# Kernel optimization log

Hardware: AMD Instinct MI355X
Metric: run time of the kernel (lower is better)

Reference implementation:

```python
import jax, jax.numpy as jnp
import numpy as np

V, E, H = 1024, 256, 512
B, L = 2048, 32
DEC_T = 7
LN_EPS = 1e-5


def _lstm(xg, Whh, h0, c0, reverse=False):
    # xg: (T, B, 4H) precomputed input gates (x @ Wih^T + b_ih + b_hh)
    def step(carry, g_in):
        h, c = carry
        g = g_in + h @ Whh.T
        i, f, gg, o = jnp.split(g, 4, axis=-1)  # torch gate order: i, f, g, o
        c = jax.nn.sigmoid(f) * c + jax.nn.sigmoid(i) * jnp.tanh(gg)
        h = jax.nn.sigmoid(o) * jnp.tanh(c)
        return (h, c), h
    (hT, cT), outs = jax.lax.scan(step, (h0, c0), xg, reverse=reverse)
    return outs, hT


def _ln(x, g, b):
    m = jnp.mean(x, axis=-1, keepdims=True)
    v = jnp.var(x, axis=-1, keepdims=True)
    return (x - m) * jax.lax.rsqrt(v + LN_EPS) * g + b


def setup_inputs() -> dict:
    key = jax.random.key(0)
    ks = jax.random.split(key, 24)
    s_e = 1.0 / np.sqrt(H)
    d = {
        'features': jax.random.randint(ks[0], (B, L), 0, V, dtype=jnp.int32),
        'eps': jax.random.normal(ks[1], (B, 1, H), dtype=jnp.float32),
        'emb': jax.random.normal(ks[2], (V, E), dtype=jnp.float32),
        'enc_Wih_f': jax.random.uniform(ks[3], (4 * H, E), minval=-s_e, maxval=s_e),
        'enc_Whh_f': jax.random.uniform(ks[4], (4 * H, H), minval=-s_e, maxval=s_e),
        'enc_bih_f': jax.random.uniform(ks[5], (4 * H,), minval=-s_e, maxval=s_e),
        'enc_bhh_f': jax.random.uniform(ks[6], (4 * H,), minval=-s_e, maxval=s_e),
        'enc_Wih_b': jax.random.uniform(ks[7], (4 * H, E), minval=-s_e, maxval=s_e),
        'enc_Whh_b': jax.random.uniform(ks[8], (4 * H, H), minval=-s_e, maxval=s_e),
        'enc_bih_b': jax.random.uniform(ks[9], (4 * H,), minval=-s_e, maxval=s_e),
        'enc_bhh_b': jax.random.uniform(ks[10], (4 * H,), minval=-s_e, maxval=s_e),
        'dec_Wih': jax.random.uniform(ks[11], (4 * H, E), minval=-s_e, maxval=s_e),
        'dec_Whh': jax.random.uniform(ks[12], (4 * H, H), minval=-s_e, maxval=s_e),
        'dec_bih': jax.random.uniform(ks[13], (4 * H,), minval=-s_e, maxval=s_e),
        'dec_bhh': jax.random.uniform(ks[14], (4 * H,), minval=-s_e, maxval=s_e),
        'mu_ln_g': jnp.ones((2 * H,)), 'mu_ln_b': jnp.zeros((2 * H,)),
        'mu_W': jax.random.uniform(ks[15], (H, 2 * H), minval=-s_e, maxval=s_e),
        'mu_b': jax.random.uniform(ks[16], (H,), minval=-s_e, maxval=s_e),
        'lv_ln_g': jnp.ones((2 * H,)), 'lv_ln_b': jnp.zeros((2 * H,)),
        'lv_W': jax.random.uniform(ks[17], (H, 2 * H), minval=-s_e, maxval=s_e) * 0.1,
        'lv_b': jax.random.uniform(ks[18], (H,), minval=-s_e, maxval=s_e),
        'ff_W': jax.random.uniform(ks[19], (V, H), minval=-s_e, maxval=s_e),
        'ff_b': jax.random.uniform(ks[20], (V,), minval=-s_e, maxval=s_e),
    }
    d['emb'] = d['emb'].at[0].set(0.0)  # padding_idx=0
    return d


def reference(features, eps, emb,
              enc_Wih_f, enc_Whh_f, enc_bih_f, enc_bhh_f,
              enc_Wih_b, enc_Whh_b, enc_bih_b, enc_bhh_b,
              dec_Wih, dec_Whh, dec_bih, dec_bhh,
              mu_ln_g, mu_ln_b, mu_W, mu_b,
              lv_ln_g, lv_ln_b, lv_W, lv_b,
              ff_W, ff_b):
    emb_eff = emb.at[0].set(0.0)  # enforce zero padding row (and zero its grad)
    x = emb_eff[features]  # (B, L, E)
    b, l, _ = x.shape
    h = dec_Whh.shape[1]
    h0 = jnp.zeros((b, h), x.dtype)

    # Bidirectional encoder: gate preactivations per direction, (L, B, 4H)
    xg_f = (jnp.einsum('ble,ge->blg', x, enc_Wih_f) + enc_bih_f + enc_bhh_f).transpose(1, 0, 2)
    xg_b = (jnp.einsum('ble,ge->blg', x, enc_Wih_b) + enc_bih_b + enc_bhh_b).transpose(1, 0, 2)
    _, hT_f = _lstm(xg_f, enc_Whh_f, h0, h0, reverse=False)
    _, hT_b = _lstm(xg_b, enc_Whh_b, h0, h0, reverse=True)
    new_h = jnp.concatenate([hT_f, hT_b], axis=-1)[:, None, :]  # (B, 1, 2H)

    mu = _ln(new_h, mu_ln_g, mu_ln_b) @ mu_W.T + mu_b          # (B, 1, H)
    logvar = _ln(new_h, lv_ln_g, lv_ln_b) @ lv_W.T + lv_b      # (B, 1, H)
    z = mu + jnp.sqrt(jnp.exp(logvar)) * eps                   # (B, 1, H)

    # Decoder: input is zeros -> input gates are just biases, broadcast over T
    gd = jnp.broadcast_to((dec_bih + dec_bhh)[None, None, :], (DEC_T, b, 4 * h))
    z0 = z[:, 0, :]
    outs, _ = _lstm(gd, dec_Whh, z0, z0, reverse=False)        # (T, B, H)
    features_hat = outs.transpose(1, 0, 2) @ ff_W.T + ff_b     # (B, T, V)
    return features, features_hat, mu, logvar
```

## Files before the change

### kernel.cpp

```cpp
#include <hip/hip_runtime.h>
#include <hip/hip_bf16.h>
#include <math.h>

#define B_ 2048
#define L_ 32
#define V_ 1024
#define E_ 256
#define H_ 512
#define DEC_T_ 7
#define NA_ (B_ * H_)

typedef unsigned short u16;
typedef unsigned int u32;
using bf16x8 = __attribute__((ext_vector_type(8))) short;
using f32x4  = __attribute__((ext_vector_type(4))) float;

#define WAITVM(n) asm volatile("s_waitcnt vmcnt(" #n ")" ::: "memory")
#define SCHED0()  __builtin_amdgcn_sched_barrier(0)

__device__ __forceinline__ u16 f2b(float f) {
  union { float f; u32 i; } x; x.f = f;
  u32 r = x.i + 0x7FFFu + ((x.i >> 16) & 1u);
  return (u16)(r >> 16);
}
__device__ __forceinline__ float b2f(u16 u) {
  union { u32 i; float f; } x; x.i = ((u32)u) << 16; return x.f;
}
__device__ __forceinline__ float sigm(float x) { return 1.f / (1.f + __expf(-x)); }
__device__ __forceinline__ float tanhfast(float x) {
  const float xx = fminf(fmaxf(x, -15.f), 15.f);
  const float e = __expf(2.f * xx);
  return (e - 1.f) / (e + 1.f);
}

__device__ __forceinline__ void gl_lds16(const void* g, void* l) {
  __builtin_amdgcn_global_load_lds((const __attribute__((address_space(1))) u32*)g,
                                   (__attribute__((address_space(3))) u32*)l, 16, 0, 0);
}
__device__ __forceinline__ void gl_lds16c(const void* g, void* l) {
  __builtin_amdgcn_global_load_lds((const __attribute__((address_space(1))) u32*)g,
                                   (__attribute__((address_space(3))) u32*)l, 16, 0, 1);
}

__device__ __forceinline__ void gbar_mono(unsigned* cnt, unsigned target) {
  __syncthreads();
  if (threadIdx.x == 0) {
    __hip_atomic_fetch_add(cnt, 1u, __ATOMIC_RELAXED, __HIP_MEMORY_SCOPE_AGENT);
    for (int it = 0; it < (1 << 20); ++it) {
      if (__hip_atomic_load(cnt, __ATOMIC_RELAXED, __HIP_MEMORY_SCOPE_AGENT) >= target) break;
      __builtin_amdgcn_s_sleep(2);
    }
  }
  asm volatile("" ::: "memory");
  __syncthreads();
}

__launch_bounds__(512, 1)
__global__ void enc_persist_k(const int* __restrict__ feat, const u16* __restrict__ emb,
                              const u16* __restrict__ Wf, const u16* __restrict__ Wbk,
                              const float* __restrict__ bsf, const float* __restrict__ bsb,
                              u16* hfa, u16* hfb, u16* hba, u16* hbb,
                              unsigned* bar) {
  __shared__ u16 Wlds[64 * 768];
  __shared__ u16 At[2][512 * 32];
  const int tid = threadIdx.x;
  const int lane = tid & 63, wave = tid >> 6;
  const int bid = blockIdx.x;
  const int xcd = bid & 7;
  const int dir = xcd >> 2;
  const int m0 = (xcd & 3) * 512;
  const int j0 = (bid >> 3) * 64;
  const u16* W = dir ? Wbk : Wf;
  const float* bsum = dir ? bsb : bsf;
  u16* hA = dir ? hba : hfa;
  u16* hB = dir ? hbb : hfb;
  unsigned* cnt = bar + xcd * 64;

  const int lr = lane & 15;
  const int swk = ((lane >> 4) ^ ((lane >> 1) & 3)) * 8;
  const int csrc = ((lane & 3) ^ ((lane >> 3) & 3)) * 8;
  const int xw = (lr >> 1) & 7;

  {
    const int row = tid >> 3;
    const u16* wsrc = W + (j0 + row) * (E_ + H_);
    u16* wdst = Wlds + row * 768;
    const int xr = (row >> 1) & 7;
#pragma unroll
    for (int q = 0; q < 12; ++q) {
      const int ck = (tid & 7) + q * 8;
      *(uint4*)(wdst + (ck ^ xr) * 8) = *(const uint4*)(wsrc + ck * 8);
    }
  }

  const int arow = lane >> 2;
  const int mbase = m0 + wave * 64;
  const int nblk = j0 >> 2;
  const int jsub = (lane >> 4) * 4;

  float creg[4][4] = {};
  __syncthreads();

  for (int s = 0; s < L_; ++s) {
    const int tc = dir ? (L_ - 1 - s) : s;
    int tok[4];
#pragma unroll
    for (int q = 0; q < 4; ++q)
      tok[q] = feat[(mbase + q * 16 + arow) * L_ + tc];
    const u16* hin = (s & 1) ? hB : hA;
    u16* hout = (s & 1) ? hA : hB;

    if (s) gbar_mono(cnt, 32u * (unsigned)s);

    auto stage = [&](int kt, int buf) {
      const int k0 = kt << 5;
      u16* ad = &At[buf][(wave * 64) * 32];
#pragma unroll
      for (int q = 0; q < 4; ++q) {
        u16* dst = ad + (q * 16) * 32;
        if (k0 < E_) gl_lds16(emb + tok[q] * E_ + k0 + csrc, dst);
        else gl_lds16c(hin + (mbase + q * 16 + arow) * H_ + (k0 - E_) + csrc, dst);
      }
    };

    f32x4 acc[4][4] = {};
    stage(0, 0);
    __syncthreads();
    int cur = 0;
    for (int kt = 0; kt < 24; ++kt) {
      if (kt + 1 < 24) stage(kt + 1, cur ^ 1);
      const u16* Ab = &At[cur][0];
      const int pk = ((kt * 4 + (lane >> 4)) ^ xw) * 8;
      bf16x8 af[4], bb[4];
#pragma unroll
      for (int t = 0; t < 4; ++t)
        af[t] = *(const bf16x8*)(Wlds + (t * 16 + lr) * 768 + pk);
#pragma unroll
      for (int t = 0; t < 4; ++t)
        bb[t] = *(const bf16x8*)(Ab + (wave * 64 + t * 16 + lr) * 32 + swk);
#pragma unroll
      for (int i = 0; i < 4; ++i)
#pragma unroll
        for (int j = 0; j < 4; ++j)
          acc[i][j] = __builtin_amdgcn_mfma_f32_16x16x32_bf16(af[i], bb[j], acc[i][j], 0, 0, 0);
      __syncthreads();
      cur ^= 1;
    }

    u16* hlds = &At[0][0];
#pragma unroll
    for (int i = 0; i < 4; ++i) {
      const int jb = j0 + i * 16 + jsub;
      const float4 bs = *(const float4*)(bsum + jb);
      const int nloc = i * 4 + (lane >> 4);
#pragma unroll
      for (int j = 0; j < 4; ++j) {
        const int mloc = wave * 64 + j * 16 + lr;
        const float gi = acc[i][j][0] + bs.x;
        const float gf = acc[i][j][1] + bs.y;
        const float gg = acc[i][j][2] + bs.z;
        const float go = acc[i][j][3] + bs.w;
        const float cn = sigm(gf) * creg[i][j] + sigm(gi) * tanhfast(gg);
        creg[i][j] = cn;
        hlds[mloc * 20 + nloc] = f2b(sigm(go) * tanhfast(cn));
      }
    }
    __syncthreads();
#pragma unroll
    for (int cc = 0; cc < 2; ++cc) {
      const int ch = tid + cc * 512;
      const int row = ch >> 1, half = ch & 1;
      *(uint4*)(hout + (m0 + row) * H_ + nblk + half * 8) =
          *(const uint4*)(hlds + row * 20 + half * 8);
    }
    __syncthreads();
  }
}

__launch_bounds__(256, 2)
__global__ void dec_persist_k(const u16* __restrict__ Wd, const float* __restrict__ bsd,
                              const u16* __restrict__ dz, const float* __restrict__ dcc,
                              u16* dech, unsigned* bar) {
  __shared__ u16 sh[4 * 8192];
  const int tid = threadIdx.x;
  const int lane = tid & 63, wave = tid >> 6;
  const int wr = wave & 1, wc = wave >> 1;
  const int bid = blockIdx.x;
  const int xcd = bid & 7;
  const int l = xcd * 32 + (bid >> 3);
  const int j0 = (l & 15) * 128;
  const int m0 = ((l >> 5) * 2 + ((l >> 4) & 1)) * 128;
  unsigned* cnt = bar + (8 + xcd) * 64;

  const int lr = lane & 15;
  const int swk = ((lane >> 4) ^ ((lane >> 1) & 3)) * 8;
  const int srow = wave * 32 + (lane >> 2);
  const int csrc = ((lane & 3) ^ ((lane >> 3) & 3)) * 8;
  const u16* wsrc0 = Wd + (j0 + srow) * H_ + csrc;
  const u16* wsrc1 = wsrc0 + 16 * H_;
  const int sw32 = (wave * 32) * 32;
  u16* hlds = sh;
  const int jb_base = j0 + wr * 64 + (lane >> 4) * 4;
  const int n0 = j0 >> 2;

  float creg[4][4];
#pragma unroll
  for (int i = 0; i < 4; ++i) {
    const int n = (jb_base + i * 16) >> 2;
#pragma unroll
    for (int j = 0; j < 4; ++j)
      creg[i][j] = dcc[n * B_ + (m0 + wc * 64 + j * 16 + lr)];
  }
  WAITVM(0);

  for (int t = 0; t < DEC_T_; ++t) {
    const u16* hin = t ? (dech + (long)(t - 1) * NA_) : dz;
    u16* hout = dech + (long)t * NA_;
    const u16* h0 = hin + (m0 + srow) * H_ + csrc;
    const u16* h1 = h0 + 16 * H_;

    if (t) gbar_mono(cnt, 32u * (unsigned)t);

    auto stage = [&](int kt) {
      const int b = kt & 3;
      const int k0 = kt << 5;
      u16* wd = sh + b * 8192 + sw32;
      u16* ad = sh + b * 8192 + 4096 + sw32;
      gl_lds16(wsrc0 + k0, wd);
      gl_lds16(wsrc1 + k0, wd + 512);
      gl_lds16c(h0 + k0, ad);
      gl_lds16c(h1 + k0, ad + 512);
    };

    f32x4 acc[4][4] = {};
    auto compute = [&](int kt) {
      const u16* Wb2 = sh + (kt & 3) * 8192;
      const u16* Ab2 = Wb2 + 4096;
      bf16x8 af[4], bb[4];
#pragma unroll
      for (int tt = 0; tt < 4; ++tt) {
        af[tt] = *(const bf16x8*)(Wb2 + (wr * 64 + tt * 16 + lr) * 32 + swk);
        bb[tt] = *(const bf16x8*)(Ab2 + (wc * 64 + tt * 16 + lr) * 32 + swk);
      }
#pragma unroll
      for (int i = 0; i < 4; ++i)
#pragma unroll
        for (int j = 0; j < 4; ++j)
          acc[i][j] = __builtin_amdgcn_mfma_f32_16x16x32_bf16(af[i], bb[j], acc[i][j], 0, 0, 0);
    };

    stage(0); stage(1); stage(2);
    for (int kt = 0; kt <= 16 - 4; ++kt) {
      WAITVM(8); SCHED0();
      __builtin_amdgcn_s_barrier(); SCHED0();
      stage(kt + 3);
      compute(kt);
    }
    WAITVM(8); SCHED0(); __builtin_amdgcn_s_barrier(); SCHED0(); compute(13);
    WAITVM(4); SCHED0(); __builtin_amdgcn_s_barrier(); SCHED0(); compute(14);
    WAITVM(0); SCHED0(); __builtin_amdgcn_s_barrier(); SCHED0(); compute(15);

#pragma unroll
    for (int i = 0; i < 4; ++i) {
      const int jb = jb_base + i * 16;
      const float4 bs = *(const float4*)(bsd + jb);
      const int nloc = (jb - j0) >> 2;
#pragma unroll
      for (int j = 0; j < 4; ++j) {
        const int mloc = wc * 64 + j * 16 + lr;
        const float gi = acc[i][j][0] + bs.x;
        const float gf = acc[i][j][1] + bs.y;
        const float gg = acc[i][j][2] + bs.z;
        const float go = acc[i][j][3] + bs.w;
        const float cn = sigm(gf) * creg[i][j] + sigm(gi) * tanhfast(gg);
        creg[i][j] = cn;
        hlds[mloc * 40 + nloc] = f2b(sigm(go) * tanhfast(cn));
      }
    }
    __syncthreads();
#pragma unroll
    for (int cc = 0; cc < 2; ++cc) {
      const int ch = tid + cc * 256;
      const int row = ch >> 2, cpos = (ch & 3) * 8;
      *(uint4*)(hout + (m0 + row) * H_ + n0 + cpos) = *(const uint4*)(hlds + row * 40 + cpos);
    }
  }
}

struct OP {
  const u16* A; const u16* W; const float* bias;
  float* Cf; int ldc; int K;
};

__launch_bounds__(256)
__global__ void out_mfma_k(OP p0, OP p1) {
  OP p = blockIdx.z ? p1 : p0;
  __shared__ u16 Ws[2][128 * 32];
  __shared__ u16 As[2][128 * 32];
  const int tid = threadIdx.x;
  const int lane = tid & 63, wave = tid >> 6;
  const int wr = wave & 1, wc = wave >> 1;
  const int v0 = blockIdx.x * 128, m0 = blockIdx.y * 128;
  const int lr = lane & 15;
  const int swk = ((lane >> 4) ^ ((lane >> 1) & 3)) * 8;

  const int srow = wave * 32 + (lane >> 2);
  const int csrc = ((lane & 3) ^ ((lane >> 3) & 3)) * 8;
  const u16* wsrc0 = p.W + (v0 + srow) * p.K + csrc;
  const u16* wsrc1 = wsrc0 + 16 * p.K;
  const u16* asrc0 = p.A + (m0 + srow) * p.K + csrc;
  const u16* asrc1 = asrc0 + 16 * p.K;
  u16* wdst0 = &Ws[0][(wave * 32) * 32];
  u16* wdst1 = wdst0 + 16 * 32;
  u16* adst0 = &As[0][(wave * 32) * 32];
  u16* adst1 = adst0 + 16 * 32;

  f32x4 acc[4][4] = {};
  const int NT = p.K >> 5;

  auto stage = [&](int kt, int buf) {
    const int k0 = kt << 5;
    const int bo = buf * 4096;
    gl_lds16(wsrc0 + k0, wdst0 + bo);
    gl_lds16(wsrc1 + k0, wdst1 + bo);
    gl_lds16(asrc0 + k0, adst0 + bo);
    gl_lds16(asrc1 + k0, adst1 + bo);
  };

  stage(0, 0);
  __syncthreads();
  int cur = 0;
  for (int kt = 0; kt < NT; ++kt) {
    if (kt + 1 < NT) stage(kt + 1, cur ^ 1);
    const u16* Wb = &Ws[cur][0];
    const u16* Ab = &As[cur][0];
    bf16x8 aa[4], bb[4];
#pragma unroll
    for (int t = 0; t < 4; ++t) {
      aa[t] = *(const bf16x8*)(Ab + (wr * 64 + t * 16 + lr) * 32 + swk);
      bb[t] = *(const bf16x8*)(Wb + (wc * 64 + t * 16 + lr) * 32 + swk);
    }
#pragma unroll
    for (int i = 0; i < 4; ++i)
#pragma unroll
      for (int j = 0; j < 4; ++j)
        acc[i][j] = __builtin_amdgcn_mfma_f32_16x16x32_bf16(aa[i], bb[j], acc[i][j], 0, 0, 0);
    __syncthreads();
    cur ^= 1;
  }

#pragma unroll
  for (int j = 0; j < 4; ++j) {
    const int v = v0 + wc * 64 + j * 16 + lr;
    const float bv = p.bias[v];
#pragma unroll
    for (int i = 0; i < 4; ++i) {
      const int mb = m0 + wr * 64 + i * 16 + (lane >> 4) * 4;
#pragma unroll
      for (int r = 0; r < 4; ++r) {
        const int m = mb + r;
        const float val = acc[i][j][r] + bv;
        if (p.ldc) p.Cf[m * p.ldc + v] = val;
        else p.Cf[(m & (B_ - 1)) * (DEC_T_ * V_) + (m >> 11) * V_ + v] = val;
      }
    }
  }
}

__global__ void prep_gates_k(const float* Wih, const float* Whh,
                             const float* b1, const float* b2,
                             u16* Wout, float* bsum, int KI, int K) {
  const int j = blockIdx.y;
  const int k = blockIdx.x * 256 + threadIdx.x;
  const int worig = (j & 3) * H_ + (j >> 2);
  const float v = (k < KI) ? Wih[worig * KI + k] : Whh[worig * H_ + (k - KI)];
  Wout[(long)j * K + k] = f2b(v);
  if (k == 0) bsum[j] = b1[worig] + b2[worig];
}

__global__ void cast_k(const float* s, u16* d) {
  const int i = blockIdx.x * 256 + threadIdx.x;
  d[i] = f2b(s[i]);
}

__global__ void init_k(u16* a, u16* b, unsigned* bar) {
  const int i = blockIdx.x * 256 + threadIdx.x;
  a[i] = 0; b[i] = 0;
  if (i < 1024) bar[i] = 0u;
}

__global__ void cast_feat_k(const int* f, float* o) {
  const int i = blockIdx.x * 256 + threadIdx.x;
  o[i] = b2f(f2b((float)f[i]));
}

__global__ void ln_k(const u16* hf, const u16* hb,
                     const float* g0, const float* b0,
                     const float* g1, const float* b1,
                     u16* A0, u16* A1) {
  const int b = blockIdx.x, t = threadIdx.x;
  const int k4 = t * 4;
  const u16* src = (k4 < H_) ? (hf + b * H_ + k4) : (hb + b * H_ + (k4 - H_));
  const ushort4 raw = *(const ushort4*)src;
  const float x0 = b2f(raw.x), x1 = b2f(raw.y), x2 = b2f(raw.z), x3 = b2f(raw.w);
  float s = x0 + x1 + x2 + x3;
  float sq = x0 * x0 + x1 * x1 + x2 * x2 + x3 * x3;
#pragma unroll
  for (int off = 32; off; off >>= 1) {
    s += __shfl_down(s, off);
    sq += __shfl_down(sq, off);
  }
  __shared__ float ss[4], ssq[4], smv[2];
  if ((t & 63) == 0) { ss[t >> 6] = s; ssq[t >> 6] = sq; }
  __syncthreads();
  if (t == 0) {
    const float S = ss[0] + ss[1] + ss[2] + ss[3];
    const float SQ = ssq[0] + ssq[1] + ssq[2] + ssq[3];
    const float m = S * (1.f / 1024.f);
    const float var = SQ * (1.f / 1024.f) - m * m;
    smv[0] = m; smv[1] = rsqrtf(var + 1e-5f);
  }
  __syncthreads();
  const float m = smv[0], rs = smv[1];
  const float4 ga = *(const float4*)(g0 + k4), ba = *(const float4*)(b0 + k4);
  const float4 gb = *(const float4*)(g1 + k4), bb = *(const float4*)(b1 + k4);
  ushort4 o0, o1;
  o0.x = f2b((x0 - m) * rs * ga.x + ba.x);
  o0.y = f2b((x1 - m) * rs * ga.y + ba.y);
  o0.z = f2b((x2 - m) * rs * ga.z + ba.z);
  o0.w = f2b((x3 - m) * rs * ga.w + ba.w);
  o1.x = f2b((x0 - m) * rs * gb.x + bb.x);
  o1.y = f2b((x1 - m) * rs * gb.y + bb.y);
  o1.z = f2b((x2 - m) * rs * gb.z + bb.z);
  o1.w = f2b((x3 - m) * rs * gb.w + bb.w);
  *(ushort4*)(A0 + b * 1024 + k4) = o0;
  *(ushort4*)(A1 + b * 1024 + k4) = o1;
}

__global__ void z_k(const float* mu, const float* lv, const float* eps,
                    u16* dz, float* dc) {
  const int i = blockIdx.x * 256 + threadIdx.x;
  const float z = mu[i] + __expf(0.5f * lv[i]) * eps[i];
  dz[i] = f2b(z);
  dc[(i & (H_ - 1)) * B_ + (i >> 9)] = z;
}

extern "C" void kernel_launch(void* const* d_in, const int* in_sizes, int n_in,
                              void* d_out, int out_size, void* d_ws, size_t ws_size,
                              hipStream_t stream) {
  const int*   features = (const int*)d_in[0];
  const float* eps      = (const float*)d_in[1];
  const float* emb      = (const float*)d_in[2];
  const float* eWih_f   = (const float*)d_in[3];
  const float* eWhh_f   = (const float*)d_in[4];
  const float* ebih_f   = (const float*)d_in[5];
  const float* ebhh_f   = (const float*)d_in[6];
  const float* eWih_b   = (const float*)d_in[7];
  const float* eWhh_b   = (const float*)d_in[8];
  const float* ebih_b   = (const float*)d_in[9];
  const float* ebhh_b   = (const float*)d_in[10];
  const float* dWhh     = (const float*)d_in[12];
  const float* dbih     = (const float*)d_in[13];
  const float* dbhh     = (const float*)d_in[14];
  const float* mu_ln_g  = (const float*)d_in[15];
  const float* mu_ln_b  = (const float*)d_in[16];
  const float* mu_W     = (const float*)d_in[17];
  const float* mu_b     = (const float*)d_in[18];
  const float* lv_ln_g  = (const float*)d_in[19];
  const float* lv_ln_b  = (const float*)d_in[20];
  const float* lv_W     = (const float*)d_in[21];
  const float* lv_b     = (const float*)d_in[22];
  const float* ff_W     = (const float*)d_in[23];
  const float* ff_b     = (const float*)d_in[24];

  float* of = (float*)d_out;
  float* o_feat = of;
  float* o_fh   = of + (B_ * L_);
  float* o_mu   = o_fh + (long)B_ * DEC_T_ * V_;
  float* o_lv   = o_mu + (long)B_ * H_;

  u16* hfa = (u16*)d_ws;
  u16* hba = hfa + NA_;
  u16* hfb = hba + NA_;
  u16* hbb = hfb + NA_;
  u16* Wenc_f = hbb + NA_;
  u16* Wenc_b = Wenc_f + 2048 * 768;
  u16* Wdec   = Wenc_b + 2048 * 768;
  u16* Wff    = Wdec + 2048 * 512;
  u16* Wmu    = Wff + 1024 * 512;
  u16* Wlv    = Wmu + 512 * 1024;
  u16* embb   = Wlv + 512 * 1024;
  float* bsum_f = (float*)(embb + V_ * E_);
  float* bsum_b = bsum_f + 2048;
  float* bsum_d = bsum_b + 2048;
  unsigned* bar = (unsigned*)(bsum_d + 2048);
  u16* dz     = (u16*)(bar + 1024);
  float* dc   = (float*)(dz + NA_);
  u16* An0    = hfb;
  u16* An1    = Wenc_f;
  u16* dech   = hfa;

  cast_feat_k<<<dim3(B_ * L_ / 256), dim3(256), 0, stream>>>(features, o_feat);
  init_k<<<dim3(NA_ / 256), dim3(256), 0, stream>>>(hfa, hba, bar);

  prep_gates_k<<<dim3(3, 2048), dim3(256), 0, stream>>>(eWih_f, eWhh_f, ebih_f, ebhh_f, Wenc_f, bsum_f, E_, E_ + H_);
  prep_gates_k<<<dim3(3, 2048), dim3(256), 0, stream>>>(eWih_b, eWhh_b, ebih_b, ebhh_b, Wenc_b, bsum_b, E_, E_ + H_);
  prep_gates_k<<<dim3(2, 2048), dim3(256), 0, stream>>>(nullptr, dWhh, dbih, dbhh, Wdec, bsum_d, 0, H_);
  cast_k<<<dim3(1024 * 512 / 256), dim3(256), 0, stream>>>(ff_W, Wff);
  cast_k<<<dim3(512 * 1024 / 256), dim3(256), 0, stream>>>(mu_W, Wmu);
  cast_k<<<dim3(512 * 1024 / 256), dim3(256), 0, stream>>>(lv_W, Wlv);
  cast_k<<<dim3(V_ * E_ / 256), dim3(256), 0, stream>>>(emb, embb);

  enc_persist_k<<<dim3(256), dim3(512), 0, stream>>>(
      features, embb, Wenc_f, Wenc_b, bsum_f, bsum_b,
      hfa, hfb, hba, hbb, bar);

  ln_k<<<dim3(B_), dim3(256), 0, stream>>>(hfa, hba, mu_ln_g, mu_ln_b, lv_ln_g, lv_ln_b, An0, An1);
  {
    OP pm{}, pl{};
    pm.A = An0; pm.W = Wmu; pm.bias = mu_b; pm.Cf = o_mu; pm.ldc = H_; pm.K = 2 * H_;
    pl = pm;
    pl.A = An1; pl.W = Wlv; pl.bias = lv_b; pl.Cf = o_lv;
    out_mfma_k<<<dim3(4, 16, 2), dim3(256), 0, stream>>>(pm, pl);
  }
  z_k<<<dim3(NA_ / 256), dim3(256), 0, stream>>>(o_mu, o_lv, eps, dz, dc);

  dec_persist_k<<<dim3(256), dim3(256), 0, stream>>>(Wdec, bsum_d, dz, dc, dech, bar);

  {
    OP po{};
    po.A = dech; po.W = Wff; po.bias = ff_b;
    po.Cf = o_fh; po.ldc = 0;
    po.K = H_;
    out_mfma_k<<<dim3(8, DEC_T_ * 16, 1), dim3(256), 0, stream>>>(po, po);
  }
}
```

Baseline: 1.057 ms.

## Give each wave private LDS staging and drop block barriers in persistent LSTM kernels

The encoder now stages activations into per-wave LDS buffers, so the K loop drops its per-step __syncthreads in favour of vmcnt/lgkmcnt waits. The grid barrier is deferred until after the embedding-part k-tiles, which read only the token embeddings, so input-projection work overlaps the wait for the other blocks' hidden states. The decoder is restructured to match: 512 threads per block, recurrent weights resident in LDS, and each wave owning 32 batch rows with wave-private staging. This removes intra-block barriers and repeated weight loads, at the cost of smaller per-wave tiles and the correctness risk of wave-local LDS reuse without block syncs.

```diff
diff --git a/kernel.cpp b/kernel.cpp
--- a/kernel.cpp
+++ b/kernel.cpp
@@ -16,6 +16,7 @@
 using f32x4  = __attribute__((ext_vector_type(4))) float;
 
 #define WAITVM(n) asm volatile("s_waitcnt vmcnt(" #n ")" ::: "memory")
+#define WAITLG0() asm volatile("s_waitcnt lgkmcnt(0)" ::: "memory")
 #define SCHED0()  __builtin_amdgcn_sched_barrier(0)
 
 __device__ __forceinline__ u16 f2b(float f) {
@@ -62,7 +63,7 @@
                               u16* hfa, u16* hfb, u16* hba, u16* hbb,
                               unsigned* bar) {
   __shared__ u16 Wlds[64 * 768];
-  __shared__ u16 At[2][512 * 32];
+  __shared__ u16 At[8][2][2048];
   const int tid = threadIdx.x;
   const int lane = tid & 63, wave = tid >> 6;
   const int bid = blockIdx.x;
@@ -76,10 +77,14 @@
   u16* hB = dir ? hbb : hfb;
   unsigned* cnt = bar + xcd * 64;
 
-  const int lr = lane & 15;
-  const int swk = ((lane >> 4) ^ ((lane >> 1) & 3)) * 8;
+  const int lr = lane & 15, hi = lane >> 4;
+  const int swk = (hi ^ ((lane >> 1) & 3)) * 8;
   const int csrc = ((lane & 3) ^ ((lane >> 3) & 3)) * 8;
   const int xw = (lr >> 1) & 7;
+  const int arow = lane >> 2;
+  const int mw0 = m0 + wave * 64;
+  const int n0 = j0 >> 2;
+  const int jsub = hi * 4;
 
   {
     const int row = tid >> 3;
@@ -92,12 +97,6 @@
       *(uint4*)(wdst + (ck ^ xr) * 8) = *(const uint4*)(wsrc + ck * 8);
     }
   }
-
-  const int arow = lane >> 2;
-  const int mbase = m0 + wave * 64;
-  const int nblk = j0 >> 2;
-  const int jsub = (lane >> 4) * 4;
-
   float creg[4][4] = {};
   __syncthreads();
 
@@ -106,183 +105,194 @@
     int tok[4];
 #pragma unroll
     for (int q = 0; q < 4; ++q)
-      tok[q] = feat[(mbase + q * 16 + arow) * L_ + tc];
+      tok[q] = feat[(mw0 + q * 16 + arow) * L_ + tc];
     const u16* hin = (s & 1) ? hB : hA;
     u16* hout = (s & 1) ? hA : hB;
 
-    if (s) gbar_mono(cnt, 32u * (unsigned)s);
-
     auto stage = [&](int kt, int buf) {
       const int k0 = kt << 5;
-      u16* ad = &At[buf][(wave * 64) * 32];
+      u16* ad = &At[wave][buf][0];
 #pragma unroll
       for (int q = 0; q < 4; ++q) {
         u16* dst = ad + (q * 16) * 32;
         if (k0 < E_) gl_lds16(emb + tok[q] * E_ + k0 + csrc, dst);
-        else gl_lds16c(hin + (mbase + q * 16 + arow) * H_ + (k0 - E_) + csrc, dst);
+        else gl_lds16c(hin + (mw0 + q * 16 + arow) * H_ + (k0 - E_) + csrc, dst);
       }
     };
 
     f32x4 acc[4][4] = {};
-    stage(0, 0);
-    __syncthreads();
-    int cur = 0;
-    for (int kt = 0; kt < 24; ++kt) {
-      if (kt + 1 < 24) stage(kt + 1, cur ^ 1);
-      const u16* Ab = &At[cur][0];
-      const int pk = ((kt * 4 + (lane >> 4)) ^ xw) * 8;
+    auto compute = [&](int kt) {
+      const int pk = ((kt * 4 + hi) ^ xw) * 8;
+      const u16* Ab = &At[wave][kt & 1][0];
       bf16x8 af[4], bb[4];
 #pragma unroll
       for (int t = 0; t < 4; ++t)
         af[t] = *(const bf16x8*)(Wlds + (t * 16 + lr) * 768 + pk);
 #pragma unroll
       for (int t = 0; t < 4; ++t)
-        bb[t] = *(const bf16x8*)(Ab + (wave * 64 + t * 16 + lr) * 32 + swk);
+        bb[t] = *(const bf16x8*)(Ab + (t * 16 + lr) * 32 + swk);
+      WAITLG0(); SCHED0();
+      if (kt + 2 < 24) stage(kt + 2, kt & 1);
 #pragma unroll
       for (int i = 0; i < 4; ++i)
 #pragma unroll
         for (int j = 0; j < 4; ++j)
           acc[i][j] = __builtin_amdgcn_mfma_f32_16x16x32_bf16(af[i], bb[j], acc[i][j], 0, 0, 0);
-      __syncthreads();
-      cur ^= 1;
-    }
-
-    u16* hlds = &At[0][0];
+    };
+
+    stage(0, 0); stage(1, 1);
+    for (int kt = 0; kt < 6; ++kt) {
+      WAITVM(4); SCHED0();
+      compute(kt);
+    }
+    if (s) gbar_mono(cnt, 32u * (unsigned)s);
+    for (int kt = 6; kt < 23; ++kt) {
+      WAITVM(4); SCHED0();
+      compute(kt);
+    }
+    WAITVM(0); SCHED0();
+    compute(23);
+
+    u16* hld = &At[wave][0][0];
 #pragma unroll
     for (int i = 0; i < 4; ++i) {
       const int jb = j0 + i * 16 + jsub;
       const float4 bs = *(const float4*)(bsum + jb);
-      const int nloc = i * 4 + (lane >> 4);
+      const int nloc = i * 4 + hi;
 #pragma unroll
       for (int j = 0; j < 4; ++j) {
-        const int mloc = wave * 64 + j * 16 + lr;
+        const int mloc = j * 16 + lr;
         const float gi = acc[i][j][0] + bs.x;
         const float gf = acc[i][j][1] + bs.y;
         const float gg = acc[i][j][2] + bs.z;
         const float go = acc[i][j][3] + bs.w;
         const float cn = sigm(gf) * creg[i][j] + sigm(gi) * tanhfast(gg);
         creg[i][j] = cn;
-        hlds[mloc * 20 + nloc] = f2b(sigm(go) * tanhfast(cn));
+        hld[mloc * 20 + nloc] = f2b(sigm(go) * tanhfast(cn));
       }
     }
-    __syncthreads();
-#pragma unroll
-    for (int cc = 0; cc < 2; ++cc) {
-      const int ch = tid + cc * 512;
-      const int row = ch >> 1, half = ch & 1;
-      *(uint4*)(hout + (m0 + row) * H_ + nblk + half * 8) =
-          *(const uint4*)(hlds + row * 20 + half * 8);
-    }
-    __syncthreads();
-  }
-}
-
-__launch_bounds__(256, 2)
+    WAITLG0(); SCHED0();
+#pragma unroll
+    for (int c = 0; c < 2; ++c) {
+      const int idx = lane + c * 64;
+      const int row = idx >> 1, half = idx & 1;
+      *(uint4*)(hout + (mw0 + row) * H_ + n0 + half * 8) =
+          *(const uint4*)(hld + row * 20 + half * 8);
+    }
+  }
+}
+
+__launch_bounds__(512, 1)
 __global__ void dec_persist_k(const u16* __restrict__ Wd, const float* __restrict__ bsd,
                               const u16* __restrict__ dz, const float* __restrict__ dcc,
                               u16* dech, unsigned* bar) {
-  __shared__ u16 sh[4 * 8192];
+  __shared__ u16 Wlds[64 * 512];
+  __shared__ u16 At[8][2][1024];
   const int tid = threadIdx.x;
   const int lane = tid & 63, wave = tid >> 6;
-  const int wr = wave & 1, wc = wave >> 1;
   const int bid = blockIdx.x;
   const int xcd = bid & 7;
-  const int l = xcd * 32 + (bid >> 3);
-  const int j0 = (l & 15) * 128;
-  const int m0 = ((l >> 5) * 2 + ((l >> 4) & 1)) * 128;
+  const int m0 = xcd * 256;
+  const int j0 = (bid >> 3) * 64;
   unsigned* cnt = bar + (8 + xcd) * 64;
 
-  const int lr = lane & 15;
-  const int swk = ((lane >> 4) ^ ((lane >> 1) & 3)) * 8;
-  const int srow = wave * 32 + (lane >> 2);
+  const int lr = lane & 15, hi = lane >> 4;
+  const int swk = (hi ^ ((lane >> 1) & 3)) * 8;
   const int csrc = ((lane & 3) ^ ((lane >> 3) & 3)) * 8;
-  const u16* wsrc0 = Wd + (j0 + srow) * H_ + csrc;
-  const u16* wsrc1 = wsrc0 + 16 * H_;
-  const int sw32 = (wave * 32) * 32;
-  u16* hlds = sh;
-  const int jb_base = j0 + wr * 64 + (lane >> 4) * 4;
+  const int xw = (lr >> 1) & 7;
+  const int arow = lane >> 2;
+  const int mw0 = m0 + wave * 32;
   const int n0 = j0 >> 2;
-
-  float creg[4][4];
+  const int jsub = hi * 4;
+
+  {
+    const int row = tid >> 3;
+    const u16* wsrc = Wd + (j0 + row) * H_;
+    u16* wdst = Wlds + row * 512;
+    const int xr = (row >> 1) & 7;
+#pragma unroll
+    for (int q = 0; q < 8; ++q) {
+      const int ck = (tid & 7) + q * 8;
+      *(uint4*)(wdst + (ck ^ xr) * 8) = *(const uint4*)(wsrc + ck * 8);
+    }
+  }
+
+  float creg[4][2];
 #pragma unroll
   for (int i = 0; i < 4; ++i) {
-    const int n = (jb_base + i * 16) >> 2;
-#pragma unroll
-    for (int j = 0; j < 4; ++j)
-      creg[i][j] = dcc[n * B_ + (m0 + wc * 64 + j * 16 + lr)];
+    const int n = (j0 + i * 16 + jsub) >> 2;
+#pragma unroll
+    for (int j = 0; j < 2; ++j)
+      creg[i][j] = dcc[n * B_ + (mw0 + j * 16 + lr)];
   }
   WAITVM(0);
+  __syncthreads();
 
   for (int t = 0; t < DEC_T_; ++t) {
     const u16* hin = t ? (dech + (long)(t - 1) * NA_) : dz;
     u16* hout = dech + (long)t * NA_;
-    const u16* h0 = hin + (m0 + srow) * H_ + csrc;
-    const u16* h1 = h0 + 16 * H_;
 
     if (t) gbar_mono(cnt, 32u * (unsigned)t);
 
-    auto stage = [&](int kt) {
-      const int b = kt & 3;
+    auto stage = [&](int kt, int buf) {
       const int k0 = kt << 5;
-      u16* wd = sh + b * 8192 + sw32;
-      u16* ad = sh + b * 8192 + 4096 + sw32;
-      gl_lds16(wsrc0 + k0, wd);
-      gl_lds16(wsrc1 + k0, wd + 512);
-      gl_lds16c(h0 + k0, ad);
-      gl_lds16c(h1 + k0, ad + 512);
+      u16* ad = &At[wave][buf][0];
+#pragma unroll
+      for (int q = 0; q < 2; ++q)
+        gl_lds16c(hin + (mw0 + q * 16 + arow) * H_ + k0 + csrc, ad + (q * 16) * 32);
     };
 
-    f32x4 acc[4][4] = {};
+    f32x4 acc[4][2] = {};
     auto compute = [&](int kt) {
-      const u16* Wb2 = sh + (kt & 3) * 8192;
-      const u16* Ab2 = Wb2 + 4096;
-      bf16x8 af[4], bb[4];
-#pragma unroll
-      for (int tt = 0; tt < 4; ++tt) {
-        af[tt] = *(const bf16x8*)(Wb2 + (wr * 64 + tt * 16 + lr) * 32 + swk);
-        bb[tt] = *(const bf16x8*)(Ab2 + (wc * 64 + tt * 16 + lr) * 32 + swk);
-      }
+      const int pk = ((kt * 4 + hi) ^ xw) * 8;
+      const u16* Ab = &At[wave][kt & 1][0];
+      bf16x8 af[4], bb[2];
+#pragma unroll
+      for (int tt = 0; tt < 4; ++tt)
+        af[tt] = *(const bf16x8*)(Wlds + (tt * 16 + lr) * 512 + pk);
+#pragma unroll
+      for (int tt = 0; tt < 2; ++tt)
+        bb[tt] = *(const bf16x8*)(Ab + (tt * 16 + lr) * 32 + swk);
+      WAITLG0(); SCHED0();
+      if (kt + 2 < 16) stage(kt + 2, kt & 1);
 #pragma unroll
       for (int i = 0; i < 4; ++i)
 #pragma unroll
-        for (int j = 0; j < 4; ++j)
+        for (int j = 0; j < 2; ++j)
           acc[i][j] = __builtin_amdgcn_mfma_f32_16x16x32_bf16(af[i], bb[j], acc[i][j], 0, 0, 0);
     };
 
-    stage(0); stage(1); stage(2);
-    for (int kt = 0; kt <= 16 - 4; ++kt) {
-      WAITVM(8); SCHED0();
-      __builtin_amdgcn_s_barrier(); SCHED0();
-      stage(kt + 3);
+    stage(0, 0); stage(1, 1);
+    for (int kt = 0; kt < 15; ++kt) {
+      WAITVM(2); SCHED0();
       compute(kt);
     }
-    WAITVM(8); SCHED0(); __builtin_amdgcn_s_barrier(); SCHED0(); compute(13);
-    WAITVM(4); SCHED0(); __builtin_amdgcn_s_barrier(); SCHED0(); compute(14);
-    WAITVM(0); SCHED0(); __builtin_amdgcn_s_barrier(); SCHED0(); compute(15);
-
+    WAITVM(0); SCHED0();
+    compute(15);
+
+    u16* hld = &At[wave][0][0];
 #pragma unroll
     for (int i = 0; i < 4; ++i) {
-      const int jb = jb_base + i * 16;
+      const int jb = j0 + i * 16 + jsub;
       const float4 bs = *(const float4*)(bsd + jb);
-      const int nloc = (jb - j0) >> 2;
-#pragma unroll
-      for (int j = 0; j < 4; ++j) {
-        const int mloc = wc * 64 + j * 16 + lr;
+      const int nloc = i * 4 + hi;
+#pragma unroll
+      for (int j = 0; j < 2; ++j) {
+        const int mloc = j * 16 + lr;
         const float gi = acc[i][j][0] + bs.x;
         const float gf = acc[i][j][1] + bs.y;
         const float gg = acc[i][j][2] + bs.z;
         const float go = acc[i][j][3] + bs.w;
         const float cn = sigm(gf) * creg[i][j] + sigm(gi) * tanhfast(gg);
         creg[i][j] = cn;
-        hlds[mloc * 40 + nloc] = f2b(sigm(go) * tanhfast(cn));
+        hld[mloc * 20 + nloc] = f2b(sigm(go) * tanhfast(cn));
       }
     }
-    __syncthreads();
-#pragma unroll
-    for (int cc = 0; cc < 2; ++cc) {
-      const int ch = tid + cc * 256;
-      const int row = ch >> 2, cpos = (ch & 3) * 8;
-      *(uint4*)(hout + (m0 + row) * H_ + n0 + cpos) = *(const uint4*)(hlds + row * 40 + cpos);
+    WAITLG0(); SCHED0();
+    {
+      const int row = lane >> 1, half = lane & 1;
+      *(uint4*)(hout + (mw0 + row) * H_ + n0 + half * 8) =
+          *(const uint4*)(hld + row * 20 + half * 8);
     }
   }
 }
@@ -525,7 +535,7 @@
   }
   z_k<<<dim3(NA_ / 256), dim3(256), 0, stream>>>(o_mu, o_lv, eps, dz, dc);
 
-  dec_persist_k<<<dim3(256), dim3(256), 0, stream>>>(Wdec, bsum_d, dz, dc, dech, bar);
+  dec_persist_k<<<dim3(256), dim3(512), 0, stream>>>(Wdec, bsum_d, dz, dc, dech, bar);
 
   {
     OP po{};
```

Measured after the change: 861.5 us. 1.23x faster.
